# Kernel optimization log

Measured on AMD Instinct MI355X. Metric: run time of the kernel, lower is better.

## Reference

```python
import jax, jax.numpy as jnp
from jax import lax
import numpy as np

N = 256              # total neurons
EPG_LO, EPG_HI = 0, 64      # epg population slice
PEN_LO, PEN_HI = 64, 128    # pen population slice (two hemispheres of 32)
HEMI = 32                    # hemisphere_length_penalty = len(pen)/2
T = 512              # Euler integration steps
B = 1024             # batch of independent trajectories
DT = 0.01            # integration step (seconds)
TAU0 = 0.02          # default time constant (seconds)


def setup_inputs() -> dict:
    key = jax.random.key(0)
    k_w, k_v, k_l = jax.random.split(key, 3)
    W = jax.random.normal(k_w, (N, N), dtype=jnp.float32) * 0.1
    log_scale = jnp.zeros((), dtype=jnp.float32)          # exp(0)=1, initial_weight_scale=1.0
    gain = jnp.ones((N,), dtype=jnp.float32)              # per-neuron gain mask (exp of per-pop params)
    bias = jnp.zeros((N,), dtype=jnp.float32)
    log_tau = jnp.full((N,), np.log(TAU0), dtype=jnp.float32)  # exp -> tau = 0.02
    velocity_scaling = jnp.float32(0.1)
    landmark_scaling = jnp.float32(0.1)
    velocity = jax.random.normal(k_v, (T, B, 2), dtype=jnp.float32)
    landmarks = jax.random.uniform(k_l, (T, B, EPG_HI - EPG_LO), dtype=jnp.float32)
    return {"W": W, "log_scale": log_scale, "gain": gain, "bias": bias,
            "log_tau": log_tau, "velocity_scaling": velocity_scaling,
            "landmark_scaling": landmark_scaling, "velocity": velocity,
            "landmarks": landmarks}


def reference(W, log_scale, gain, bias, log_tau, velocity_scaling,
              landmark_scaling, velocity, landmarks):
    # Effective recurrent weights: sum over blocks of exp(scale)*masked block
    # collapses to exp(log_scale) * W when all block scalings are tied.
    W_eff = jnp.exp(log_scale) * W                      # [N, N]
    tau = jnp.exp(log_tau)                              # [N]
    coef = DT / tau                                     # [N] Euler dt/tau

    def step(state, xs):                                # state: [B, N]
        v, lm = xs                                      # v: [B, 2], lm: [B, 64]
        ext = jnp.zeros((B, N), dtype=state.dtype)
        # landmark input -> epg neurons
        ext = ext.at[:, EPG_LO:EPG_HI].set(lm * landmark_scaling)
        # angular velocity -> pen neurons, split by hemisphere
        ext = ext.at[:, PEN_LO:PEN_LO + HEMI].set(v[:, :1] * velocity_scaling)
        ext = ext.at[:, PEN_LO + HEMI:PEN_HI].set(v[:, 1:2] * velocity_scaling)
        total = state @ W_eff + ext                     # [B, N]
        rate = jax.nn.relu(gain * total + bias)
        new_state = state + coef * (rate - state)       # leaky Euler update
        return new_state, None

    state0 = jnp.zeros((B, N), dtype=jnp.float32)
    final, _ = lax.scan(step, state0, (velocity, landmarks))
    return final[:, EPG_LO:EPG_HI]                      # epg output, [B, 64]
```

## Files before the change

kernel.cpp:

```cpp
#include <hip/hip_runtime.h>

#define NN 256
#define TT 512
#define BB 1024
#define DTC 0.01f

typedef _Float16 half8 __attribute__((ext_vector_type(8)));
typedef float f32x4 __attribute__((ext_vector_type(4)));

__device__ __forceinline__ f32x4 mfma_z(half8 a, half8 b) {
  f32x4 d;
  asm("v_mfma_f32_16x16x32_f16 %0, %1, %2, 0" : "=v"(d) : "a"(a), "v"(b));
  return d;
}
__device__ __forceinline__ void mfma_p(f32x4& c, half8 a, half8 b) {
  asm("v_mfma_f32_16x16x32_f16 %0, %1, %2, %0" : "+v"(c) : "a"(a), "v"(b));
}

template <int CTRL>
__device__ __forceinline__ float rormax(float x) {
  int yi = __builtin_amdgcn_update_dpp(0, __float_as_int(x), CTRL, 0xf, 0xf, false);
  return fmaxf(x, __int_as_float(yi));
}

__global__ __launch_bounds__(256, 1) void ring_attractor_kernel(
    const float* __restrict__ W, const float* __restrict__ log_scale,
    const float* __restrict__ gain, const float* __restrict__ bias,
    const float* __restrict__ log_tau, const float* __restrict__ vscale_p,
    const float* __restrict__ lscale_p, const float* __restrict__ velocity,
    const float* __restrict__ landmarks, float* __restrict__ out) {
  __shared__ __align__(16) _Float16 fragH[2][4096];
  __shared__ __align__(16) _Float16 fragL[2][4096];
  __shared__ __align__(16) float maxslot[2][4];

  const int tid = threadIdx.x;
  const int w  = tid >> 6;
  const int l  = tid & 63;
  const int g  = l >> 4;
  const int li = l & 15;
  const int br = blockIdx.x * 16 + li;

  const float es  = expf(log_scale[0]);
  const float vs  = vscale_p[0];
  const float lms = lscale_p[0];

  float gain_r[4][4], bias_r[4][4], coef_r[4][4];
#pragma unroll
  for (int nt = 0; nt < 4; ++nt)
#pragma unroll
    for (int q = 0; q < 4; ++q) {
      int c = w * 64 + nt * 16 + g * 4 + q;
      gain_r[nt][q] = gain[c];
      bias_r[nt][q] = bias[c];
      coef_r[nt][q] = DTC / expf(log_tau[c]);
    }

  half8 whi[4][8], wlo[4][8];
#pragma unroll
  for (int nt = 0; nt < 4; ++nt)
#pragma unroll
    for (int ks = 0; ks < 8; ++ks) {
      half8 hi, lo;
#pragma unroll
      for (int j = 0; j < 8; ++j) {
        int k = ks * 32 + g * 4 + (j & 3) + ((j >> 2) << 4);
        int m = w * 64 + nt * 16 + li;
        float wv = W[k * NN + m] * es;
        _Float16 h = (_Float16)wv;
        hi[j] = h;
        lo[j] = (_Float16)(wv - (float)h);
      }
      whi[nt][ks] = hi;
      wlo[nt][ks] = lo;
    }

  float s_r[4][4];
#pragma unroll
  for (int nt = 0; nt < 4; ++nt)
#pragma unroll
    for (int q = 0; q < 4; ++q) s_r[nt][q] = 0.f;

  const int wb0 = ((w * 2 + 0) * 64 + g * 16 + li) * 8;
  const int wb1 = ((w * 2 + 1) * 64 + g * 16 + li) * 8;
  {
    half8 z;
#pragma unroll
    for (int j = 0; j < 8; ++j) z[j] = (_Float16)0.f;
    *reinterpret_cast<half8*>(&fragH[0][wb0]) = z;
    *reinterpret_cast<half8*>(&fragH[0][wb1]) = z;
    *reinterpret_cast<half8*>(&fragL[0][wb0]) = z;
    *reinterpret_cast<half8*>(&fragL[0][wb1]) = z;
    if (tid < 8) maxslot[tid >> 2][tid & 3] = 0.f;
  }
  float inv_scale = 1.f;
  float amPrev = 0.f;

  f32x4 eA0{}, eA1{}, eA2{}, eA3{}, eB0{}, eB1{}, eB2{}, eB3{};
  if (w == 0) {
    const float* p = landmarks + (size_t)br * 64 + g * 4;
    eA0 = *reinterpret_cast<const f32x4*>(p);
    eA1 = *reinterpret_cast<const f32x4*>(p + 16);
    eA2 = *reinterpret_cast<const f32x4*>(p + 32);
    eA3 = *reinterpret_cast<const f32x4*>(p + 48);
  } else if (w == 1) {
    const float* p = velocity + (size_t)br * 2;
    eA0[0] = p[0];
    eA0[1] = p[1];
  }
  __syncthreads();

#define TAIL(NT, AH, AL, AC, E0, E1, E2, E3)                                   \
  {                                                                            \
    f32x4 av = (AH + AL) + AC;                                                 \
    _Pragma("unroll")                                                          \
    for (int q = 0; q < 4; ++q) {                                              \
      float ext;                                                               \
      if (w == 0) {                                                            \
        f32x4 ev = (NT == 0) ? E0 : (NT == 1) ? E1 : (NT == 2) ? E2 : E3;      \
        ext = lms * ev[q];                                                     \
      } else if (w == 1) {                                                     \
        ext = vs * ((NT < 2) ? E0[0] : E0[1]);                                 \
      } else {                                                                 \
        ext = 0.f;                                                             \
      }                                                                        \
      float tot = __builtin_fmaf(av[q], inv_scale, ext);                       \
      float rate = fmaxf(__builtin_fmaf(gain_r[NT][q], tot, bias_r[NT][q]),    \
                         0.f);                                                 \
      float sv = s_r[NT][q];                                                   \
      sv = __builtin_fmaf(coef_r[NT][q], rate - sv, sv);                       \
      s_r[NT][q] = sv;                                                         \
      am = fmaxf(am, fabsf(sv));                                               \
    }                                                                          \
  }

#define STEP(T, CUR, E0, E1, E2, E3, P0, P1, P2, P3)                           \
  {                                                                            \
      \
    {                                                                          \
      float r = amPrev;                                                        \
      r = rormax<0x121>(r);                                                    \
      r = rormax<0x122>(r);                                                    \
      r = rormax<0x124>(r);                                                    \
      r = rormax<0x128>(r);                                                    \
      r = fmaxf(r, __shfl_xor(r, 16));                                         \
      r = fmaxf(r, __shfl_xor(r, 32));                                         \
      if (l == 0) maxslot[CUR][w] = r;                                         \
    }                                                                          \
           \
    float scale_n, inv_n;                                                      \
    {                                                                          \
      f32x4 mv = *reinterpret_cast<const f32x4*>(&maxslot[CUR ^ 1][0]);        \
      float M = fmaxf(fmaxf(mv[0], mv[1]), fmaxf(mv[2], mv[3]));               \
      int e = 134 - (int)(__float_as_uint(M) >> 23);                           \
      e = e > 9 ? 9 : e;                                                       \
      scale_n = __int_as_float((e + 127) << 23);                               \
      inv_n = __int_as_float((127 - e) << 23);                                 \
    }                                                                          \
                                     \
    {                                                                          \
      const int tn = (T) + 1 < TT ? (T) + 1 : TT - 1;                          \
      if (w == 0) {                                                            \
        const float* p = landmarks + ((size_t)tn * BB + br) * 64 + g * 4;      \
        P0 = *reinterpret_cast<const f32x4*>(p);                               \
        P1 = *reinterpret_cast<const f32x4*>(p + 16);                          \
        P2 = *reinterpret_cast<const f32x4*>(p + 32);                          \
        P3 = *reinterpret_cast<const f32x4*>(p + 48);                          \
      } else if (w == 1) {                                                     \
        const float* p = velocity + ((size_t)tn * BB + br) * 2;                \
        P0[0] = p[0];                                                          \
        P0[1] = p[1];                                                          \
      }                                                                        \
    }                                                                          \
         \
    half8 bhr[8], blr[8];                                                      \
    _Pragma("unroll")                                                          \
    for (int ks = 0; ks < 8; ++ks) {                                           \
      const int rb = (ks * 64 + g * 16 + li) * 8;                              \
      bhr[ks] = *reinterpret_cast<const half8*>(&fragH[CUR][rb]);              \
      blr[ks] = *reinterpret_cast<const half8*>(&fragL[CUR][rb]);              \
    }                                                                          \
                   \
    f32x4 a0h, a1h, a2h, a3h, a0l, a1l, a2l, a3l, a0c, a1c, a2c, a3c;          \
    a0h = mfma_z(whi[0][0], bhr[0]);                                           \
    a1h = mfma_z(whi[1][0], bhr[0]);                                           \
    a2h = mfma_z(whi[2][0], bhr[0]);                                           \
    a3h = mfma_z(whi[3][0], bhr[0]);                                           \
    a0l = mfma_z(wlo[0][0], bhr[0]);                                           \
    a1l = mfma_z(wlo[1][0], bhr[0]);                                           \
    a2l = mfma_z(wlo[2][0], bhr[0]);                                           \
    a3l = mfma_z(wlo[3][0], bhr[0]);                                           \
    a0c = mfma_z(whi[0][0], blr[0]);                                           \
    a1c = mfma_z(whi[1][0], blr[0]);                                           \
    a2c = mfma_z(whi[2][0], blr[0]);                                           \
    a3c = mfma_z(whi[3][0], blr[0]);                                           \
    _Pragma("unroll")                                                          \
    for (int ks = 1; ks < 7; ++ks) {                                           \
      mfma_p(a0h, whi[0][ks], bhr[ks]);                                        \
      mfma_p(a1h, whi[1][ks], bhr[ks]);                                        \
      mfma_p(a2h, whi[2][ks], bhr[ks]);                                        \
      mfma_p(a3h, whi[3][ks], bhr[ks]);                                        \
      mfma_p(a0l, wlo[0][ks], bhr[ks]);                                        \
      mfma_p(a1l, wlo[1][ks], bhr[ks]);                                        \
      mfma_p(a2l, wlo[2][ks], bhr[ks]);                                        \
      mfma_p(a3l, wlo[3][ks], bhr[ks]);                                        \
      mfma_p(a0c, whi[0][ks], blr[ks]);                                        \
      mfma_p(a1c, whi[1][ks], blr[ks]);                                        \
      mfma_p(a2c, whi[2][ks], blr[ks]);                                        \
      mfma_p(a3c, whi[3][ks], blr[ks]);                                        \
    }                                                                          \
               \
    float am = 0.f;                                                            \
    mfma_p(a0h, whi[0][7], bhr[7]);                                            \
    mfma_p(a0l, wlo[0][7], bhr[7]);                                            \
    mfma_p(a0c, whi[0][7], blr[7]);                                            \
    mfma_p(a1h, whi[1][7], bhr[7]);                                            \
    mfma_p(a1l, wlo[1][7], bhr[7]);                                            \
    mfma_p(a1c, whi[1][7], blr[7]);                                            \
    asm volatile("s_nop 7" : "+v"(a0h), "+v"(a0l), "+v"(a0c));                 \
    TAIL(0, a0h, a0l, a0c, E0, E1, E2, E3)                                     \
    mfma_p(a2h, whi[2][7], bhr[7]);                                            \
    mfma_p(a2l, wlo[2][7], bhr[7]);                                            \
    mfma_p(a2c, whi[2][7], blr[7]);                                            \
    TAIL(1, a1h, a1l, a1c, E0, E1, E2, E3)                                     \
    mfma_p(a3h, whi[3][7], bhr[7]);                                            \
    mfma_p(a3l, wlo[3][7], bhr[7]);                                            \
    mfma_p(a3c, whi[3][7], blr[7]);                                            \
            \
    {                                                                          \
      half8 h0, l0;                                                            \
      _Pragma("unroll")                                                        \
      for (int j = 0; j < 8; ++j) {                                            \
        float sc0 = s_r[j >> 2][j & 3] * scale_n;                              \
        _Float16 q0 = (_Float16)sc0;                                           \
        h0[j] = q0;                                                            \
        l0[j] = (_Float16)(sc0 - (float)q0);                                   \
      }                                                                        \
      *reinterpret_cast<half8*>(&fragH[CUR ^ 1][wb0]) = h0;                    \
      *reinterpret_cast<half8*>(&fragL[CUR ^ 1][wb0]) = l0;                    \
    }                                                                          \
    TAIL(2, a2h, a2l, a2c, E0, E1, E2, E3)                                     \
    asm volatile("s_nop 7" : "+v"(a3h), "+v"(a3l), "+v"(a3c));                 \
    TAIL(3, a3h, a3l, a3c, E0, E1, E2, E3)                                     \
                                      \
    {                                                                          \
      half8 h1, l1;                                                            \
      _Pragma("unroll")                                                        \
      for (int j = 0; j < 8; ++j) {                                            \
        float sc1 = s_r[2 + (j >> 2)][j & 3] * scale_n;                        \
        _Float16 q1 = (_Float16)sc1;                                           \
        h1[j] = q1;                                                            \
        l1[j] = (_Float16)(sc1 - (float)q1);                                   \
      }                                                                        \
      *reinterpret_cast<half8*>(&fragH[CUR ^ 1][wb1]) = h1;                    \
      *reinterpret_cast<half8*>(&fragL[CUR ^ 1][wb1]) = l1;                    \
    }                                                                          \
    amPrev = am;                                                               \
    inv_scale = inv_n;                                                         \
    __syncthreads();                                                           \
  }

#pragma unroll 1
  for (int t = 0; t < TT; t += 2) {
    STEP(t, 0, eA0, eA1, eA2, eA3, eB0, eB1, eB2, eB3)
    STEP(t + 1, 1, eB0, eB1, eB2, eB3, eA0, eA1, eA2, eA3)
  }
#undef STEP
#undef TAIL

  if (w == 0) {
#pragma unroll
    for (int nt = 0; nt < 4; ++nt) {
      f32x4 o;
#pragma unroll
      for (int q = 0; q < 4; ++q) o[q] = s_r[nt][q];
      *reinterpret_cast<f32x4*>(out + (size_t)br * 64 + nt * 16 + g * 4) = o;
    }
  }
}

extern "C" void kernel_launch(void* const* d_in, const int* in_sizes, int n_in,
                              void* d_out, int out_size, void* d_ws, size_t ws_size,
                              hipStream_t stream) {
  const float* W         = (const float*)d_in[0];
  const float* log_scale = (const float*)d_in[1];
  const float* gain      = (const float*)d_in[2];
  const float* bias      = (const float*)d_in[3];
  const float* log_tau   = (const float*)d_in[4];
  const float* vscale    = (const float*)d_in[5];
  const float* lscale    = (const float*)d_in[6];
  const float* velocity  = (const float*)d_in[7];
  const float* landmarks = (const float*)d_in[8];
  float* out = (float*)d_out;

  ring_attractor_kernel<<<dim3(BB / 16), dim3(256), 0, stream>>>(
      W, log_scale, gain, bias, log_tau, vscale, lscale, velocity, landmarks, out);
}
```

Baseline: 684.3 us.

## Interleave LDS fragment reads with MFMA chain and load inputs within step

New measurement: 724.1 us. 1.06x slower.

```diff
diff --git a/kernel.cpp b/kernel.cpp
--- a/kernel.cpp
+++ b/kernel.cpp
@@ -94,32 +94,53 @@
   }
   float inv_scale = 1.f;
   float amPrev = 0.f;
-
-  f32x4 eA0{}, eA1{}, eA2{}, eA3{}, eB0{}, eB1{}, eB2{}, eB3{};
-  if (w == 0) {
-    const float* p = landmarks + (size_t)br * 64 + g * 4;
-    eA0 = *reinterpret_cast<const f32x4*>(p);
-    eA1 = *reinterpret_cast<const f32x4*>(p + 16);
-    eA2 = *reinterpret_cast<const f32x4*>(p + 32);
-    eA3 = *reinterpret_cast<const f32x4*>(p + 48);
-  } else if (w == 1) {
-    const float* p = velocity + (size_t)br * 2;
-    eA0[0] = p[0];
-    eA0[1] = p[1];
-  }
   __syncthreads();
 
-#define TAIL(NT, AH, AL, AC, E0, E1, E2, E3)                                   \
+#define RD(CUR, KS, BH, BL)                                                    \
+  {                                                                            \
+    const int rb = ((KS) * 64 + g * 16 + li) * 8;                              \
+    BH = *reinterpret_cast<const half8*>(&fragH[CUR][rb]);                     \
+    BL = *reinterpret_cast<const half8*>(&fragL[CUR][rb]);                     \
+  }
+
+#define K12(KS, BH, BL)                                                        \
+  mfma_p(a0h, whi[0][KS], BH);                                                 \
+  mfma_p(a1h, whi[1][KS], BH);                                                 \
+  mfma_p(a2h, whi[2][KS], BH);                                                 \
+  mfma_p(a3h, whi[3][KS], BH);                                                 \
+  mfma_p(a0l, wlo[0][KS], BH);                                                 \
+  mfma_p(a1l, wlo[1][KS], BH);                                                 \
+  mfma_p(a2l, wlo[2][KS], BH);                                                 \
+  mfma_p(a3l, wlo[3][KS], BH);                                                 \
+  mfma_p(a0c, whi[0][KS], BL);                                                 \
+  mfma_p(a1c, whi[1][KS], BL);                                                 \
+  mfma_p(a2c, whi[2][KS], BL);                                                 \
+  mfma_p(a3c, whi[3][KS], BL);
+#define K12Z(KS, BH, BL)                                                       \
+  a0h = mfma_z(whi[0][KS], BH);                                                \
+  a1h = mfma_z(whi[1][KS], BH);                                                \
+  a2h = mfma_z(whi[2][KS], BH);                                                \
+  a3h = mfma_z(whi[3][KS], BH);                                                \
+  a0l = mfma_z(wlo[0][KS], BH);                                                \
+  a1l = mfma_z(wlo[1][KS], BH);                                                \
+  a2l = mfma_z(wlo[2][KS], BH);                                                \
+  a3l = mfma_z(wlo[3][KS], BH);                                                \
+  a0c = mfma_z(whi[0][KS], BL);                                                \
+  a1c = mfma_z(whi[1][KS], BL);                                                \
+  a2c = mfma_z(whi[2][KS], BL);                                                \
+  a3c = mfma_z(whi[3][KS], BL);
+
+#define TAIL(NT, AH, AL, AC)                                                   \
   {                                                                            \
     f32x4 av = (AH + AL) + AC;                                                 \
     _Pragma("unroll")                                                          \
     for (int q = 0; q < 4; ++q) {                                              \
       float ext;                                                               \
       if (w == 0) {                                                            \
-        f32x4 ev = (NT == 0) ? E0 : (NT == 1) ? E1 : (NT == 2) ? E2 : E3;      \
+        f32x4 ev = (NT == 0) ? lm0 : (NT == 1) ? lm1 : (NT == 2) ? lm2 : lm3;  \
         ext = lms * ev[q];                                                     \
       } else if (w == 1) {                                                     \
-        ext = vs * ((NT < 2) ? E0[0] : E0[1]);                                 \
+        ext = vs * ((NT < 2) ? vv0 : vv1);                                     \
       } else {                                                                 \
         ext = 0.f;                                                             \
       }                                                                        \
@@ -133,7 +154,9 @@
     }                                                                          \
   }
 
-#define STEP(T, CUR, E0, E1, E2, E3, P0, P1, P2, P3)                           \
+#define SB() __builtin_amdgcn_sched_barrier(0)
+
+#define STEP(T, CUR)                                                           \
   {                                                                            \
       \
     {                                                                          \
@@ -156,76 +179,60 @@
       scale_n = __int_as_float((e + 127) << 23);                               \
       inv_n = __int_as_float((127 - e) << 23);                                 \
     }                                                                          \
-                                     \
-    {                                                                          \
-      const int tn = (T) + 1 < TT ? (T) + 1 : TT - 1;                          \
-      if (w == 0) {                                                            \
-        const float* p = landmarks + ((size_t)tn * BB + br) * 64 + g * 4;      \
-        P0 = *reinterpret_cast<const f32x4*>(p);                               \
-        P1 = *reinterpret_cast<const f32x4*>(p + 16);                          \
-        P2 = *reinterpret_cast<const f32x4*>(p + 32);                          \
-        P3 = *reinterpret_cast<const f32x4*>(p + 48);                          \
-      } else if (w == 1) {                                                     \
-        const float* p = velocity + ((size_t)tn * BB + br) * 2;                \
-        P0[0] = p[0];                                                          \
-        P0[1] = p[1];                                                          \
-      }                                                                        \
-    }                                                                          \
          \
-    half8 bhr[8], blr[8];                                                      \
-    _Pragma("unroll")                                                          \
-    for (int ks = 0; ks < 8; ++ks) {                                           \
-      const int rb = (ks * 64 + g * 16 + li) * 8;                              \
-      bhr[ks] = *reinterpret_cast<const half8*>(&fragH[CUR][rb]);              \
-      blr[ks] = *reinterpret_cast<const half8*>(&fragL[CUR][rb]);              \
-    }                                                                          \
-                   \
+    f32x4 lm0{}, lm1{}, lm2{}, lm3{};                                          \
+    float vv0 = 0.f, vv1 = 0.f;                                                \
+    if (w == 0) {                                                              \
+      const float* p = landmarks + ((size_t)(T)*BB + br) * 64 + g * 4;         \
+      lm0 = *reinterpret_cast<const f32x4*>(p);                                \
+      lm1 = *reinterpret_cast<const f32x4*>(p + 16);                           \
+      lm2 = *reinterpret_cast<const f32x4*>(p + 32);                           \
+      lm3 = *reinterpret_cast<const f32x4*>(p + 48);                           \
+    } else if (w == 1) {                                                       \
+      const float* p = velocity + ((size_t)(T)*BB + br) * 2;                   \
+      vv0 = p[0];                                                              \
+      vv1 = p[1];                                                              \
+    }                                                                          \
+            \
+    half8 bh0, bl0, bh1, bl1, bh2, bl2, bh3, bl3;                              \
     f32x4 a0h, a1h, a2h, a3h, a0l, a1l, a2l, a3l, a0c, a1c, a2c, a3c;          \
-    a0h = mfma_z(whi[0][0], bhr[0]);                                           \
-    a1h = mfma_z(whi[1][0], bhr[0]);                                           \
-    a2h = mfma_z(whi[2][0], bhr[0]);                                           \
-    a3h = mfma_z(whi[3][0], bhr[0]);                                           \
-    a0l = mfma_z(wlo[0][0], bhr[0]);                                           \
-    a1l = mfma_z(wlo[1][0], bhr[0]);                                           \
-    a2l = mfma_z(wlo[2][0], bhr[0]);                                           \
-    a3l = mfma_z(wlo[3][0], bhr[0]);                                           \
-    a0c = mfma_z(whi[0][0], blr[0]);                                           \
-    a1c = mfma_z(whi[1][0], blr[0]);                                           \
-    a2c = mfma_z(whi[2][0], blr[0]);                                           \
-    a3c = mfma_z(whi[3][0], blr[0]);                                           \
-    _Pragma("unroll")                                                          \
-    for (int ks = 1; ks < 7; ++ks) {                                           \
-      mfma_p(a0h, whi[0][ks], bhr[ks]);                                        \
-      mfma_p(a1h, whi[1][ks], bhr[ks]);                                        \
-      mfma_p(a2h, whi[2][ks], bhr[ks]);                                        \
-      mfma_p(a3h, whi[3][ks], bhr[ks]);                                        \
-      mfma_p(a0l, wlo[0][ks], bhr[ks]);                                        \
-      mfma_p(a1l, wlo[1][ks], bhr[ks]);                                        \
-      mfma_p(a2l, wlo[2][ks], bhr[ks]);                                        \
-      mfma_p(a3l, wlo[3][ks], bhr[ks]);                                        \
-      mfma_p(a0c, whi[0][ks], blr[ks]);                                        \
-      mfma_p(a1c, whi[1][ks], blr[ks]);                                        \
-      mfma_p(a2c, whi[2][ks], blr[ks]);                                        \
-      mfma_p(a3c, whi[3][ks], blr[ks]);                                        \
-    }                                                                          \
-               \
+    RD(CUR, 0, bh0, bl0)                                                       \
+    RD(CUR, 1, bh1, bl1)                                                       \
+    SB();                                                                      \
+    RD(CUR, 2, bh2, bl2)                                                       \
+    RD(CUR, 3, bh3, bl3)                                                       \
+    K12Z(0, bh0, bl0)                                                          \
+    K12(1, bh1, bl1)                                                           \
+    SB();                                                                      \
+    RD(CUR, 4, bh0, bl0)                                                       \
+    RD(CUR, 5, bh1, bl1)                                                       \
+    K12(2, bh2, bl2)                                                           \
+    K12(3, bh3, bl3)                                                           \
+    SB();                                                                      \
+    RD(CUR, 6, bh2, bl2)                                                       \
+    RD(CUR, 7, bh3, bl3)                                                       \
+    K12(4, bh0, bl0)                                                           \
+    K12(5, bh1, bl1)                                                           \
+    SB();                                                                      \
+          \
     float am = 0.f;                                                            \
-    mfma_p(a0h, whi[0][7], bhr[7]);                                            \
-    mfma_p(a0l, wlo[0][7], bhr[7]);                                            \
-    mfma_p(a0c, whi[0][7], blr[7]);                                            \
-    mfma_p(a1h, whi[1][7], bhr[7]);                                            \
-    mfma_p(a1l, wlo[1][7], bhr[7]);                                            \
-    mfma_p(a1c, whi[1][7], blr[7]);                                            \
+    K12(6, bh2, bl2)                                                           \
+    mfma_p(a0h, whi[0][7], bh3);                                               \
+    mfma_p(a0l, wlo[0][7], bh3);                                               \
+    mfma_p(a0c, whi[0][7], bl3);                                               \
+    mfma_p(a1h, whi[1][7], bh3);                                               \
+    mfma_p(a1l, wlo[1][7], bh3);                                               \
+    mfma_p(a1c, whi[1][7], bl3);                                               \
     asm volatile("s_nop 7" : "+v"(a0h), "+v"(a0l), "+v"(a0c));                 \
-    TAIL(0, a0h, a0l, a0c, E0, E1, E2, E3)                                     \
-    mfma_p(a2h, whi[2][7], bhr[7]);                                            \
-    mfma_p(a2l, wlo[2][7], bhr[7]);                                            \
-    mfma_p(a2c, whi[2][7], blr[7]);                                            \
-    TAIL(1, a1h, a1l, a1c, E0, E1, E2, E3)                                     \
-    mfma_p(a3h, whi[3][7], bhr[7]);                                            \
-    mfma_p(a3l, wlo[3][7], bhr[7]);                                            \
-    mfma_p(a3c, whi[3][7], blr[7]);                                            \
-            \
+    TAIL(0, a0h, a0l, a0c)                                                     \
+    mfma_p(a2h, whi[2][7], bh3);                                               \
+    mfma_p(a2l, wlo[2][7], bh3);                                               \
+    mfma_p(a2c, whi[2][7], bl3);                                               \
+    TAIL(1, a1h, a1l, a1c)                                                     \
+    mfma_p(a3h, whi[3][7], bh3);                                               \
+    mfma_p(a3l, wlo[3][7], bh3);                                               \
+    mfma_p(a3c, whi[3][7], bl3);                                               \
+                 \
     {                                                                          \
       half8 h0, l0;                                                            \
       _Pragma("unroll")                                                        \
@@ -238,10 +245,10 @@
       *reinterpret_cast<half8*>(&fragH[CUR ^ 1][wb0]) = h0;                    \
       *reinterpret_cast<half8*>(&fragL[CUR ^ 1][wb0]) = l0;                    \
     }                                                                          \
-    TAIL(2, a2h, a2l, a2c, E0, E1, E2, E3)                                     \
+    TAIL(2, a2h, a2l, a2c)                                                     \
     asm volatile("s_nop 7" : "+v"(a3h), "+v"(a3l), "+v"(a3c));                 \
-    TAIL(3, a3h, a3l, a3c, E0, E1, E2, E3)                                     \
-                                      \
+    TAIL(3, a3h, a3l, a3c)                                                     \
+                                           \
     {                                                                          \
       half8 h1, l1;                                                            \
       _Pragma("unroll")                                                        \
@@ -261,11 +268,15 @@
 
 #pragma unroll 1
   for (int t = 0; t < TT; t += 2) {
-    STEP(t, 0, eA0, eA1, eA2, eA3, eB0, eB1, eB2, eB3)
-    STEP(t + 1, 1, eB0, eB1, eB2, eB3, eA0, eA1, eA2, eA3)
+    STEP(t, 0)
+    STEP(t + 1, 1)
   }
 #undef STEP
 #undef TAIL
+#undef K12
+#undef K12Z
+#undef RD
+#undef SB
 
   if (w == 0) {
 #pragma unroll
```
